# Optimization experiments

Measured on AMD Instinct MI355X. Metric: run time of the kernel, lower is better.

Reference implementation:

```python
import jax, jax.numpy as jnp
import numpy as np
from jax.scipy.special import gammaln

# sizes (see shape_source)
N_CELLS = 1024
N_GENES = 1000
N_LATENT = 50
NB_ENC = 16          # encoder histogram bins per gene
NB_DEC = 16          # decoder mixture components (sum(n_decoder_bins))
N_HID = 16           # encoder hidden dim
N_CUTS = 4_000_000
N_FRAGS = 2_000_000
N_TOTAL_CELLS = 10_000
N_TOTAL_CUTS = 50_000_000
BN_EPS = 1e-5


def _normal_logprob(x, loc, scale):
    z = (x - loc) / scale
    return -0.5 * z * z - jnp.log(scale) - 0.5 * jnp.log(2.0 * jnp.pi)


def setup_inputs() -> dict:
    key = jax.random.key(0)
    ks = jax.random.split(key, 20)
    cut_coordinates = jax.random.uniform(ks[0], (N_CUTS,), dtype=jnp.float32)
    cut_cell = jax.random.randint(ks[1], (N_CUTS,), 0, N_CELLS)
    cut_local_gene_ix = jax.random.randint(ks[2], (N_CUTS,), 0, N_GENES)
    cut_local_cellxgene_ix = cut_cell * N_GENES + cut_local_gene_ix
    local_cellxgene_ix = jax.random.randint(ks[3], (N_FRAGS,), 0, N_CELLS * N_GENES)
    genes_oi = jnp.arange(N_GENES)
    cells_oi = jnp.arange(N_CELLS)
    eps = jax.random.normal(ks[4], (N_CELLS, N_LATENT), dtype=jnp.float32)
    n_in = N_GENES * NB_ENC
    enc_W1 = jax.random.normal(ks[5], (n_in, N_HID)) * (1.0 / np.sqrt(n_in))
    enc_b1 = jnp.zeros((N_HID,))
    bn_gamma = jnp.ones((N_HID,))
    bn_beta = jnp.zeros((N_HID,))
    W_loc = jax.random.normal(ks[6], (N_HID, N_LATENT)) * (1.0 / np.sqrt(N_HID))
    b_loc = jnp.zeros((N_LATENT,))
    W_scale = jax.random.normal(ks[7], (N_HID, N_LATENT)) * (1.0 / np.sqrt(N_HID))
    b_scale = jnp.zeros((N_LATENT,))
    logit_weight = jax.random.normal(ks[8], (N_GENES, N_LATENT, NB_DEC)) * 0.05
    rho_weight = jax.random.normal(ks[9], (N_GENES, N_LATENT)) * 0.05
    baseline_heights = jax.random.normal(ks[10], (N_GENES, NB_DEC)) * 0.1
    libsize = jax.random.randint(ks[11], (N_TOTAL_CELLS,), 1000, 20000)
    rho_bias = jax.random.uniform(ks[12], (N_GENES,), minval=1e-4, maxval=1e-2)
    return dict(
        cut_coordinates=cut_coordinates, eps=eps,
        enc_W1=enc_W1, enc_b1=enc_b1, bn_gamma=bn_gamma, bn_beta=bn_beta,
        W_loc=W_loc, b_loc=b_loc, W_scale=W_scale, b_scale=b_scale,
        logit_weight=logit_weight, rho_weight=rho_weight,
        baseline_heights=baseline_heights, rho_bias=rho_bias,
        cut_local_cellxgene_ix=cut_local_cellxgene_ix,
        cut_local_gene_ix=cut_local_gene_ix,
        local_cellxgene_ix=local_cellxgene_ix,
        genes_oi=genes_oi, cells_oi=cells_oi, libsize=libsize,
    )


def reference(cut_coordinates, eps, enc_W1, enc_b1, bn_gamma, bn_beta,
              W_loc, b_loc, W_scale, b_scale, logit_weight, rho_weight,
              baseline_heights, rho_bias, cut_local_cellxgene_ix,
              cut_local_gene_ix, local_cellxgene_ix, genes_oi, cells_oi,
              libsize):
    n_cells = cells_oi.shape[0]
    n_genes = genes_oi.shape[0]

    # ---- Encoder: digitize + bincount histogram ----
    bin_enc = jnp.minimum(jnp.floor(cut_coordinates * NB_ENC), NB_ENC - 1).astype(jnp.int32)
    digitized = bin_enc + cut_local_cellxgene_ix.astype(jnp.int32) * NB_ENC
    counts = jax.ops.segment_sum(jnp.ones_like(cut_coordinates), digitized,
                                 num_segments=n_cells * n_genes * NB_ENC)
    x = jnp.log1p(counts.reshape(n_cells, n_genes * NB_ENC))  # [C, G*NB]

    h = x @ enc_W1 + enc_b1
    mu = h.mean(axis=0)
    var = h.var(axis=0)  # biased, matches torch BN in train mode
    h = (h - mu) / jnp.sqrt(var + BN_EPS) * bn_gamma + bn_beta
    h = jax.nn.relu(h)
    loc = h @ W_loc + b_loc                 # [C, L]
    scale = jnp.exp(h @ W_scale + b_scale)  # [C, L]

    # ---- latent sample + KL ----
    q_scale = scale * 0.1
    latent = loc + q_scale * eps
    latent_kl = (_normal_logprob(latent, 0.0, 1.0)
                 - _normal_logprob(latent, loc, q_scale)) * (N_TOTAL_CELLS / n_cells)

    # ---- Decoder (n_layers=0: per-gene linear heads) ----
    lw = logit_weight[genes_oi]                       # [G, L, K]
    rw = rho_weight[genes_oi]                         # [G, L]
    mixture_delta = jnp.einsum('cl,glk->cgk', latent, lw)  # [C, G, K]
    rho_delta = jnp.einsum('cl,gl->cg', latent, rw)        # [C, G]
    md_cxg = mixture_delta.reshape(n_cells * n_genes, NB_DEC)
    md_cut = md_cxg[cut_local_cellxgene_ix]           # [N_CUTS, K] gather
    mixture_delta_kl = _normal_logprob(lw, 0.0, 0.1)

    # ---- mixture likelihood: piecewise-constant spline density per cut ----
    logits = baseline_heights[cut_local_gene_ix] + md_cut  # [N_CUTS, K]
    logp = jax.nn.log_softmax(logits, axis=-1)
    bin_dec = jnp.minimum(jnp.floor(cut_coordinates * NB_DEC), NB_DEC - 1).astype(jnp.int32)
    likelihood_mixture = (jnp.take_along_axis(logp, bin_dec[:, None], axis=1)[:, 0]
                          + jnp.log(float(NB_DEC)))

    # ---- fragment-count Poisson likelihood ----
    fragexpr = (rho_bias[genes_oi][None, :] * jnp.exp(rho_delta)
                * libsize[cells_oi].astype(jnp.float32)[:, None])  # [C, G]
    fragmentcounts = jax.ops.segment_sum(
        jnp.ones((local_cellxgene_ix.shape[0],), jnp.float32),
        local_cellxgene_ix, num_segments=n_cells * n_genes
    ).reshape(n_cells, n_genes)
    likelihood_frag = (fragmentcounts * jnp.log(fragexpr) - fragexpr
                       - gammaln(fragmentcounts + 1.0))

    rho_delta_kl = _normal_logprob(rw, 0.0, 0.1)

    likelihood = (likelihood_mixture.sum() * (N_TOTAL_CUTS / cut_coordinates.shape[0])
                  + likelihood_frag.sum() * (N_TOTAL_CELLS / n_cells))
    elbo = (-likelihood - latent_kl.sum() - mixture_delta_kl.sum()
            - rho_delta_kl.sum())
    return elbo
```

## Files before the change

kernel.cpp:

```cpp
#include <hip/hip_runtime.h>
#include <hip/hip_bf16.h>
#include <math.h>


#define G_      1000
#define C_      1024
#define L_      50
#define K_      16
#define NHID_   16
#define CUT_SCALE   12.5f
#define CELL_SCALE  9.765625f

#define CHUNK_    6144
#define RCAP_CUT  18432
#define RCAP_FRAG 9216

#define NPB_MIX  4000
#define NPB_POIS 4000
#define NPB_WKL  256
#define NPB_TOT  8456

#define GCNTC_OFF  0ull
#define GCNTF_OFF  1024ull
#define ZERO_BYTES 2048ull
#define BNSUM_OFF  2048ull
#define LATBF_OFF  2304ull
#define LWT_OFF    133376ull
#define ENTC_OFF   2181376ull
#define ENTF_OFF   11618560ull
#define MERGED_OFF 16337152ull
#define FRAGU8_OFF 24529152ull
#define P_OFF      25577728ull
#define HT_OFF     29772032ull
#define LATT_OFF   29837568ull
#define PB_OFF     30042368ull
#define WS_NEED    30076192ull

typedef __attribute__((ext_vector_type(8))) short short8;
typedef __attribute__((ext_vector_type(4))) float f32x4;

__device__ __constant__ float LGT[32] = {
    0.0f, 0.0f, 0.6931471805599453f, 1.791759469228055f, 3.1780538303479458f,
    4.787491742782046f, 6.579251212010101f, 8.525161361065415f,
    10.60460290274525f, 12.801827480081469f, 15.104412573075516f,
    17.502307845873887f, 19.987214495661885f, 22.552163853123425f,
    25.19122118273868f, 27.89927138384089f, 30.671860106080672f,
    33.50507345013689f, 36.39544520803305f, 39.339884187199495f,
    42.335616460753485f, 45.38013889847691f, 48.47118135183523f,
    51.60667556776438f, 54.78472939811232f, 58.00360522298052f,
    61.261701761002f, 64.55753862700633f, 67.88974313718154f,
    71.25703896716801f, 74.65823634883016f, 78.0922235533153f };

__device__ __forceinline__ float block_sum_256(float v) {
    __shared__ float sm[256];
    int t = threadIdx.x;
    __syncthreads();
    sm[t] = v;
    __syncthreads();
#pragma unroll
    for (int s = 128; s > 0; s >>= 1) {
        if (t < s) sm[t] += sm[t + s];
        __syncthreads();
    }
    return sm[0];
}

__global__ __launch_bounds__(256)
void part_kernel(const int* __restrict__ cut_ix,
                 const float* __restrict__ coord,
                 const int* __restrict__ frag_ix,
                 unsigned int* __restrict__ gcnt_c,
                 unsigned int* __restrict__ gcnt_f,
                 unsigned short* __restrict__ entc,
                 unsigned short* __restrict__ entf,
                 const float* __restrict__ lw,
                 const float* __restrict__ rw,
                 __hip_bfloat16* __restrict__ lwT,
                 float* __restrict__ pb_wkl,
                 int n_cuts, int n_frags, int ncc, int nblk_part) {
    int t = threadIdx.x;
    int bid = blockIdx.x;
    if (bid >= nblk_part) {
        int r = bid - nblk_part;
        if (r < 256) {
            for (int g = r; g < G_; g += 256) {
                for (int i = t; i < L_ * K_; i += 256) {
                    float v = lw[(size_t)g * (L_ * K_) + i];
                    lwT[(size_t)g * 1024 + (i & 15) * 64 + (i >> 4)] =
                        __float2bfloat16(v);
                }
                for (int i = t; i < 16 * 14; i += 256) {
                    int n = i / 14, l = 50 + (i % 14);
                    lwT[(size_t)g * 1024 + n * 64 + l] = __float2bfloat16(0.f);
                }
            }
        } else {
            const int NTOT = G_ * L_ * K_ + G_ * L_;
            int wb = r - 256;
            float s = 0.f;
            for (int i = wb * 256 + t; i < NTOT; i += 256 * 256) {
                float w = (i < G_ * L_ * K_) ? lw[i] : rw[i - G_ * L_ * K_];
                s += fmaf(-50.f * w, w, 1.3836465597893733f);
            }
            s = block_sum_256(s);
            if (t == 0) pb_wkl[wb] = -s;
        }
        return;
    }
    __shared__ unsigned int cnt[256], excl[256], cur[256], gbas[256];
    __shared__ unsigned short stage[CHUNK_];
    __shared__ unsigned char bkof[CHUNK_];
    bool isCut = (bid < ncc);
    int blk = isCut ? bid : bid - ncc;
    const int* idx = isCut ? cut_ix : frag_ix;
    int n = isCut ? n_cuts : n_frags;
    int rcap = isCut ? RCAP_CUT : RCAP_FRAG;
    unsigned int* gcount = isCut ? gcnt_c : gcnt_f;
    unsigned short* ent = isCut ? entc : entf;
    int i0 = blk * CHUNK_;
    cnt[t] = 0;
    int4 I[6]; float4 X[6];
    unsigned int vm;
    bool full = (i0 + CHUNK_ <= n);
    if (full) {
        const int4* ip = (const int4*)(idx + i0);
#pragma unroll
        for (int k = 0; k < 6; ++k) I[k] = ip[k * 256 + t];
        if (isCut) {
            const float4* xp = (const float4*)(coord + i0);
#pragma unroll
            for (int k = 0; k < 6; ++k) X[k] = xp[k * 256 + t];
        }
        vm = 0xFFFFFFu;
    } else {
        vm = 0;
#pragma unroll
        for (int k = 0; k < 6; ++k) {
            int r0 = i0 + (k * 256 + t) * 4;
            int* Ii = (int*)&I[k]; float* Xi = (float*)&X[k];
#pragma unroll
            for (int u = 0; u < 4; ++u) {
                bool v = (r0 + u) < n;
                if (v) vm |= 1u << (k * 4 + u);
                Ii[u] = v ? idx[r0 + u] : 0;
                Xi[u] = (v && isCut) ? coord[r0 + u] : 0.f;
            }
        }
    }
    __syncthreads();
#pragma unroll
    for (int k = 0; k < 6; ++k) {
        const int* Ii = (const int*)&I[k];
        const float* Xi = (const float*)&X[k];
#pragma unroll
        for (int u = 0; u < 4; ++u) {
            if (vm & (1u << (k * 4 + u))) {
                int ix = Ii[u];
                int c = ix / G_;
                int g = ix - c * G_;
                unsigned int bk;
                if (isCut) {
                    int b = (int)(Xi[u] * 16.f); b = b > 15 ? 15 : b;
                    bk = ((unsigned)(c >> 6) << 4) | ((unsigned)(g * K_ + b) >> 10);
                } else {
                    bk = ((unsigned)(c >> 6) << 4) | ((unsigned)g >> 6);
                }
                atomicAdd(&cnt[bk], 1u);
            }
        }
    }
    __syncthreads();
    excl[t] = cnt[t];
    __syncthreads();
    for (int o = 1; o < 256; o <<= 1) {
        unsigned int v = (t >= o) ? excl[t - o] : 0u;
        __syncthreads();
        excl[t] += v;
        __syncthreads();
    }
    unsigned int my_excl = excl[t] - cnt[t];
    gbas[t] = cnt[t] ? atomicAdd(&gcount[t], cnt[t]) : 0u;
    cur[t] = my_excl;
    __syncthreads();
    excl[t] = my_excl;
    __syncthreads();
#pragma unroll
    for (int k = 0; k < 6; ++k) {
        const int* Ii = (const int*)&I[k];
        const float* Xi = (const float*)&X[k];
#pragma unroll
        for (int u = 0; u < 4; ++u) {
            if (vm & (1u << (k * 4 + u))) {
                int ix = Ii[u];
                int c = ix / G_;
                int g = ix - c * G_;
                unsigned int bk; unsigned short e;
                if (isCut) {
                    int b = (int)(Xi[u] * 16.f); b = b > 15 ? 15 : b;
                    int bin = g * K_ + b;
                    bk = ((unsigned)(c >> 6) << 4) | ((unsigned)bin >> 10);
                    e = (unsigned short)(((c & 63) << 10) | (bin & 1023));
                } else {
                    bk = ((unsigned)(c >> 6) << 4) | ((unsigned)g >> 6);
                    e = (unsigned short)(((c & 63) << 6) | (g & 63));
                }
                unsigned int p = atomicAdd(&cur[bk], 1u);
                stage[p] = e;
                bkof[p] = (unsigned char)bk;
            }
        }
    }
    __syncthreads();
    int total = n - i0; if (total > CHUNK_) total = CHUNK_;
    for (int p = t; p < total; p += 256) {
        unsigned int bk = bkof[p];
        unsigned int dst = gbas[bk] + (p - excl[bk]);
        if (dst < (unsigned)rcap)
            ent[(size_t)bk * rcap + dst] = stage[p];
    }
}

__global__ __launch_bounds__(256)
void mid_kernel(const unsigned int* __restrict__ gcnt_c,
                const unsigned short* __restrict__ entc,
                const unsigned int* __restrict__ gcnt_f,
                const unsigned short* __restrict__ entf,
                const float* __restrict__ W1,
                unsigned int* __restrict__ merged,
                unsigned int* __restrict__ fragw,
                float* __restrict__ P) {
    __shared__ unsigned int h[4096];
    __shared__ float w1s[4096];
    int t = threadIdx.x;
    int bid = blockIdx.x;
    if (bid < 1024) {
        int bk = bid >> 2, q = bid & 3;
        int cg = bk >> 4, bc = bk & 15;
        int wbase = (bc * 1024 + q * 256) * NHID_;
#pragma unroll
        for (int r = 0; r < 16; ++r) {
            int i = r * 256 + t;
            int gi = wbase + i;
            w1s[i] = (gi < 16000 * NHID_) ? W1[gi] : 0.f;
        }
        for (int i = t; i < 2048; i += 256) h[i] = 0;
        __syncthreads();
        unsigned int count = gcnt_c[bk];
        if (count > RCAP_CUT) count = RCAP_CUT;
        const unsigned int* e32 = (const unsigned int*)(entc + (size_t)bk * RCAP_CUT);
        unsigned int npair = count >> 1;
        for (unsigned int base = 0; base < npair; base += 1024) {
            unsigned int w[4]; bool val[4];
#pragma unroll
            for (int u = 0; u < 4; ++u) {
                unsigned int p = base + u * 256 + t;
                val[u] = (p < npair);
                w[u] = val[u] ? e32[p] : 0u;
            }
#pragma unroll
            for (int u = 0; u < 4; ++u) {
                if (val[u]) {
                    unsigned int v0 = w[u] & 0xffffu, v1 = w[u] >> 16;
                    unsigned int b0 = v0 & 1023u, b1 = v1 & 1023u;
                    if ((int)(b0 >> 8) == q) {
                        unsigned int c0 = v0 >> 10;
                        atomicAdd(&h[(b0 & 255u) * 8 + (c0 >> 3)],
                                  1u << ((c0 & 7) * 4));
                    }
                    if ((int)(b1 >> 8) == q) {
                        unsigned int c1 = v1 >> 10;
                        atomicAdd(&h[(b1 & 255u) * 8 + (c1 >> 3)],
                                  1u << ((c1 & 7) * 4));
                    }
                }
            }
        }
        if (t == 0 && (count & 1u)) {
            unsigned int v = ((const unsigned short*)e32)[count - 1];
            unsigned int b0 = v & 1023u;
            if ((int)(b0 >> 8) == q) {
                unsigned int c0 = v >> 10;
                atomicAdd(&h[(b0 & 255u) * 8 + (c0 >> 3)], 1u << ((c0 & 7) * 4));
            }
        }
        __syncthreads();
        for (int i = t; i < 2048; i += 256) {
            int bin = bc * 1024 + q * 256 + (i >> 3);
            if (bin < 16000)
                merged[(unsigned)bin * 128u + (unsigned)cg * 8u + (i & 7)] = h[i];
        }
        int c_lo = t & 63, sub = t >> 6;
        float acc[NHID_];
#pragma unroll
        for (int j = 0; j < NHID_; ++j) acc[j] = 0.f;
        int rbase = bc * 1024 + q * 256 + sub * 64;
        int sh = (c_lo & 7) * 4;
        const float4* w1v = (const float4*)w1s;
#pragma unroll 2
        for (int bl = 0; bl < 64; ++bl) {
            int row = rbase + bl;
            if (row < 16000) {
                int rl = sub * 64 + bl;
                unsigned int w = h[rl * 8 + (c_lo >> 3)];
                float xv = __logf((float)(((w >> sh) & 0xfu) + 1u));
                float4 wa = w1v[rl * 4 + 0];
                float4 wb = w1v[rl * 4 + 1];
                float4 wc = w1v[rl * 4 + 2];
                float4 wd = w1v[rl * 4 + 3];
                acc[0] = fmaf(xv, wa.x, acc[0]);  acc[1] = fmaf(xv, wa.y, acc[1]);
                acc[2] = fmaf(xv, wa.z, acc[2]);  acc[3] = fmaf(xv, wa.w, acc[3]);
                acc[4] = fmaf(xv, wb.x, acc[4]);  acc[5] = fmaf(xv, wb.y, acc[5]);
                acc[6] = fmaf(xv, wb.z, acc[6]);  acc[7] = fmaf(xv, wb.w, acc[7]);
                acc[8] = fmaf(xv, wc.x, acc[8]);  acc[9] = fmaf(xv, wc.y, acc[9]);
                acc[10] = fmaf(xv, wc.z, acc[10]); acc[11] = fmaf(xv, wc.w, acc[11]);
                acc[12] = fmaf(xv, wd.x, acc[12]); acc[13] = fmaf(xv, wd.y, acc[13]);
                acc[14] = fmaf(xv, wd.z, acc[14]); acc[15] = fmaf(xv, wd.w, acc[15]);
            }
        }
        __syncthreads();
        float* sp = (float*)h;
#pragma unroll
        for (int j = 0; j < NHID_; ++j) sp[sub * 1024 + j * 64 + c_lo] = acc[j];
        __syncthreads();
        for (int i = t; i < 1024; i += 256) {
            int j = i >> 6, c = i & 63;
            float v = sp[j * 64 + c] + sp[1024 + j * 64 + c]
                    + sp[2048 + j * 64 + c] + sp[3072 + j * 64 + c];
            P[(size_t)((bc * 4 + q) * NHID_ + j) * C_ + cg * 64 + c] = v;
        }
    } else {
        int bk = bid - 1024, cg = bk >> 4, gc = bk & 15;
        for (int i = t; i < 2048; i += 256) h[i] = 0;
        __syncthreads();
        unsigned int count = gcnt_f[bk];
        if (count > RCAP_FRAG) count = RCAP_FRAG;
        const unsigned short* e = entf + (size_t)bk * RCAP_FRAG;
#pragma unroll 4
        for (unsigned int p = t; p < count; p += 256) {
            unsigned int v = e[p];
            unsigned int g_lo = v & 63u;
            unsigned int c_lo = v >> 6;
            atomicAdd(&h[g_lo * 32 + (c_lo >> 1)], 1u << ((c_lo & 1) * 16));
        }
        __syncthreads();
        for (int i = t; i < 1024; i += 256) {
            int g_lo = i >> 4, wb = i & 15;
            unsigned int lo = h[g_lo * 32 + wb * 2];
            unsigned int hi = h[g_lo * 32 + wb * 2 + 1];
            unsigned int outv = (lo & 0xffu) | (((lo >> 16) & 0xffu) << 8)
                              | ((hi & 0xffu) << 16) | (((hi >> 16) & 0xffu) << 24);
            int g = gc * 64 + g_lo;
            if (g < G_)
                fragw[(unsigned)g * 256u + (unsigned)cg * 16u + wb] = outv;
        }
    }
}

__global__ __launch_bounds__(256)
void bn_kernel(const float* __restrict__ P,
               float* __restrict__ hT,
               double* __restrict__ bnsum) {
    int j = blockIdx.x;
    int t = threadIdx.x;
    float s1 = 0.f, s2 = 0.f;
#pragma unroll
    for (int u = 0; u < 4; ++u) {
        int c = u * 256 + t;
        float s = 0.f;
#pragma unroll 8
        for (int ch = 0; ch < 64; ++ch)
            s += P[(size_t)(ch * NHID_ + j) * C_ + c];
        hT[j * C_ + c] = s;
        s1 += s; s2 += s * s;
    }
    s1 = block_sum_256(s1);
    s2 = block_sum_256(s2);
    if (t == 0) { bnsum[j] = (double)s1; bnsum[NHID_ + j] = (double)s2; }
}

__global__ __launch_bounds__(256)
void latent_kernel(const float* __restrict__ hT,
                   const double* __restrict__ bnsum,
                   const float* __restrict__ gamma,
                   const float* __restrict__ beta,
                   const float* __restrict__ W_loc,
                   const float* __restrict__ b_loc,
                   const float* __restrict__ W_scale,
                   const float* __restrict__ b_scale,
                   const float* __restrict__ eps,
                   float* __restrict__ latT,
                   __hip_bfloat16* __restrict__ latbf,
                   float* __restrict__ pb) {
    int idx = blockIdx.x * 256 + threadIdx.x;
    float kl = 0.f;
    {
        int c = idx / L_;
        int l = idx - c * L_;
        float hb[NHID_];
#pragma unroll
        for (int j = 0; j < NHID_; ++j) {
            float mean = (float)(bnsum[j] * (1.0 / C_));
            float ex2  = (float)(bnsum[NHID_ + j] * (1.0 / C_));
            float var = ex2 - mean * mean;
            float rstd = rsqrtf(var + 1e-5f);
            float sc = gamma[j] * rstd;
            float sh = beta[j] - mean * sc;
            float v = fmaf(hT[j * C_ + c], sc, sh);
            hb[j] = v > 0.f ? v : 0.f;
        }
        float loc = b_loc[l], ls = b_scale[l];
#pragma unroll
        for (int j = 0; j < NHID_; ++j) {
            loc = fmaf(hb[j], W_loc[j * L_ + l], loc);
            ls  = fmaf(hb[j], W_scale[j * L_ + l], ls);
        }
        float qs = 0.1f * __expf(ls);
        float e = eps[idx];
        float lat = fmaf(qs, e, loc);
        latT[(size_t)l * C_ + c] = lat;
        latbf[c * 64 + l] = __float2bfloat16(lat);
        if (l < 14) latbf[c * 64 + 50 + l] = __float2bfloat16(0.f);
        float z = (lat - loc) / qs;
        kl = fmaf(-0.5f * lat, lat, fmaf(0.5f * z, z, __logf(qs)));
    }
    float s = block_sum_256(kl);
    if (threadIdx.x == 0) pb[blockIdx.x] = -CELL_SCALE * s;
}

__global__ __launch_bounds__(256)
void mixpois_kernel(const __hip_bfloat16* __restrict__ latbf,
                    const __hip_bfloat16* __restrict__ lwT,
                    const unsigned int* __restrict__ merged,
                    const float* __restrict__ baseline,
                    const float* __restrict__ latT,
                    const float* __restrict__ rw,
                    const float* __restrict__ rho_bias,
                    const int* __restrict__ libsize,
                    const unsigned char* __restrict__ fragb,
                    float* __restrict__ pb) {
    int g = blockIdx.x;
    if (blockIdx.y < 4) {
        int lane = threadIdx.x & 63;
        int wv = threadIdx.x >> 6;
        int n = lane & 15;
        int quad = lane >> 4;
        const __hip_bfloat16* bb = lwT + (size_t)g * 1024 + n * 64 + quad * 8;
        short8 b1 = *(const short8*)bb;
        short8 b2 = *(const short8*)(bb + 32);
        float bl = baseline[g * K_ + n];
        float partial = 0.f;
        int cwave = blockIdx.y * 256 + wv * 64;
#pragma unroll
        for (int mt = 0; mt < 4; ++mt) {
            int c0 = cwave + mt * 16;
            const __hip_bfloat16* aa = latbf + (size_t)(c0 + n) * 64 + quad * 8;
            short8 a1 = *(const short8*)aa;
            short8 a2 = *(const short8*)(aa + 32);
            f32x4 d = {bl, bl, bl, bl};
            d = __builtin_amdgcn_mfma_f32_16x16x32_bf16(a1, b1, d, 0, 0, 0);
            d = __builtin_amdgcn_mfma_f32_16x16x32_bf16(a2, b2, d, 0, 0, 0);
            float mx[4], ex[4];
#pragma unroll
            for (int r = 0; r < 4; ++r) mx[r] = d[r];
#pragma unroll
            for (int m = 1; m < 16; m <<= 1)
#pragma unroll
                for (int r = 0; r < 4; ++r)
                    mx[r] = fmaxf(mx[r], __shfl_xor(mx[r], m));
#pragma unroll
            for (int r = 0; r < 4; ++r) ex[r] = __expf(d[r] - mx[r]);
#pragma unroll
            for (int m = 1; m < 16; m <<= 1)
#pragma unroll
                for (int r = 0; r < 4; ++r) ex[r] += __shfl_xor(ex[r], m);
            int cp = c0 + quad * 4;
            unsigned int hw =
                merged[(unsigned)(g * K_ + n) * 128u + ((unsigned)cp >> 3)];
            int sb = (cp & 7) * 4;
#pragma unroll
            for (int r = 0; r < 4; ++r) {
                float lse = mx[r] + __logf(ex[r]);
                float cnt = (float)((hw >> (sb + r * 4)) & 0xfu);
                partial = fmaf(cnt, d[r] - lse, partial);
            }
        }
        float s = block_sum_256(-CUT_SCALE * partial);
        if (threadIdx.x == 0) pb[blockIdx.y * G_ + g] = s;
    } else {
        int yc = blockIdx.y - 4;
        int c = yc * 256 + threadIdx.x;
        const float* rwg = rw + (size_t)g * L_;
        float rho = 0.f;
#pragma unroll 10
        for (int l = 0; l < L_; ++l)
            rho = fmaf(latT[l * C_ + c], rwg[l], rho);
        unsigned int fc = fragb[(size_t)g * C_ + c];
        float fe = rho_bias[g] * __expf(rho) * (float)libsize[c];
        float lf = fmaf((float)fc, __logf(fe), -fe) - LGT[fc > 31u ? 31u : fc];
        float s = block_sum_256(-CELL_SCALE * lf);
        if (threadIdx.x == 0) pb[NPB_MIX + yc * G_ + g] = s;
    }
}

__global__ __launch_bounds__(256)
void final_kernel(const float* __restrict__ pb, float* __restrict__ out) {
    __shared__ double sm[256];
    int t = threadIdx.x;
    double a = 0.0;
    for (int i = t; i < NPB_TOT; i += 256) a += (double)pb[i];
    sm[t] = a;
    __syncthreads();
#pragma unroll
    for (int s = 128; s > 0; s >>= 1) {
        if (t < s) sm[t] += sm[t + s];
        __syncthreads();
    }
    if (t == 0) out[0] = (float)(sm[0] - 138629436.11198905);
}

extern "C" void kernel_launch(void* const* d_in, const int* in_sizes, int n_in,
                              void* d_out, int out_size, void* d_ws, size_t ws_size,
                              hipStream_t stream) {
    const float* cut_coord = (const float*)d_in[0];
    const float* eps       = (const float*)d_in[1];
    const float* enc_W1    = (const float*)d_in[2];
    const float* bn_gamma  = (const float*)d_in[4];
    const float* bn_beta   = (const float*)d_in[5];
    const float* W_loc     = (const float*)d_in[6];
    const float* b_loc     = (const float*)d_in[7];
    const float* W_scale   = (const float*)d_in[8];
    const float* b_scale   = (const float*)d_in[9];
    const float* logit_w   = (const float*)d_in[10];
    const float* rho_w     = (const float*)d_in[11];
    const float* baseline  = (const float*)d_in[12];
    const float* rho_bias  = (const float*)d_in[13];
    const int* cut_cxg     = (const int*)d_in[14];
    const int* frag_ix     = (const int*)d_in[16];
    const int* libsize     = (const int*)d_in[19];

    int n_cuts  = in_sizes[0];
    int n_frags = in_sizes[16];

    char* ws = (char*)d_ws;
    unsigned int*   gcnt_c = (unsigned int*)(ws + GCNTC_OFF);
    unsigned int*   gcnt_f = (unsigned int*)(ws + GCNTF_OFF);
    double*         bnsum  = (double*)(ws + BNSUM_OFF);
    __hip_bfloat16* latbf  = (__hip_bfloat16*)(ws + LATBF_OFF);
    __hip_bfloat16* lwT    = (__hip_bfloat16*)(ws + LWT_OFF);
    unsigned short* entc   = (unsigned short*)(ws + ENTC_OFF);
    unsigned short* entf   = (unsigned short*)(ws + ENTF_OFF);
    unsigned int*   merged = (unsigned int*)(ws + MERGED_OFF);
    unsigned int*   fragw  = (unsigned int*)(ws + FRAGU8_OFF);
    float*          P      = (float*)(ws + P_OFF);
    float*          hT     = (float*)(ws + HT_OFF);
    float*          latT   = (float*)(ws + LATT_OFF);
    float*          pb     = (float*)(ws + PB_OFF);
    float*          out    = (float*)d_out;

    int ncc = (n_cuts + CHUNK_ - 1) / CHUNK_;
    int ncf = (n_frags + CHUNK_ - 1) / CHUNK_;
    int nblk_part = ncc + ncf;

    hipMemsetAsync(ws, 0, ZERO_BYTES, stream);

    part_kernel<<<nblk_part + 512, 256, 0, stream>>>(
        cut_cxg, cut_coord, frag_ix, gcnt_c, gcnt_f, entc, entf,
        logit_w, rho_w, lwT, pb + NPB_MIX + NPB_POIS,
        n_cuts, n_frags, ncc, nblk_part);
    mid_kernel<<<1280, 256, 0, stream>>>(
        gcnt_c, entc, gcnt_f, entf, enc_W1, merged, fragw, P);
    bn_kernel<<<NHID_, 256, 0, stream>>>(P, hT, bnsum);
    latent_kernel<<<(C_ * L_) / 256, 256, 0, stream>>>(
        hT, bnsum, bn_gamma, bn_beta, W_loc, b_loc, W_scale, b_scale,
        eps, latT, latbf, pb + NPB_MIX + NPB_POIS + NPB_WKL);
    mixpois_kernel<<<dim3(G_, 8), 256, 0, stream>>>(
        latbf, lwT, merged, baseline, latT, rho_w, rho_bias, libsize,
        (const unsigned char*)fragw, pb);
    final_kernel<<<1, 256, 0, stream>>>(pb, out);
}
```

Baseline: 244.6 us.

## Fold BN and final reduction into neighbouring kernels; atomic-accumulate encoder hidden sums

Removes bn_kernel by having mid_kernel atomically add its partial hidden activations straight into hT, and each latent_kernel block recomputes the batch-norm statistics itself. final_kernel is merged into mixpois_kernel using a two-level done counter, so the last block performs the final sum. The bucket prefix scan becomes a wavefront shuffle scan, and W1 is read from global memory with a wave-uniform address instead of being staged in LDS. The changes cut kernel launches, the P round trip and LDS usage. In exchange they add float atomics with nondeterministic summation order, redundant BN statistics work in every latent block, and a last-block completion protocol.

After: 369.5 us. 1.51x slower.

```diff
diff --git a/kernel.cpp b/kernel.cpp
--- a/kernel.cpp
+++ b/kernel.cpp
@@ -22,19 +22,18 @@
 
 #define GCNTC_OFF  0ull
 #define GCNTF_OFF  1024ull
-#define ZERO_BYTES 2048ull
-#define BNSUM_OFF  2048ull
-#define LATBF_OFF  2304ull
-#define LWT_OFF    133376ull
-#define ENTC_OFF   2181376ull
-#define ENTF_OFF   11618560ull
-#define MERGED_OFF 16337152ull
-#define FRAGU8_OFF 24529152ull
-#define P_OFF      25577728ull
-#define HT_OFF     29772032ull
-#define LATT_OFF   29837568ull
-#define PB_OFF     30042368ull
-#define WS_NEED    30076192ull
+#define DONE_OFF   2048ull
+#define HT_OFF     18688ull
+#define ZERO_BYTES 84224ull
+#define LATBF_OFF  84224ull
+#define LWT_OFF    215296ull
+#define ENTC_OFF   2263296ull
+#define ENTF_OFF   11700480ull
+#define MERGED_OFF 16419072ull
+#define FRAGU8_OFF 24611072ull
+#define LATT_OFF   25635072ull
+#define PB_OFF     25839872ull
+#define WS_NEED    25873696ull
 
 typedef __attribute__((ext_vector_type(8))) short short8;
 typedef __attribute__((ext_vector_type(4))) float f32x4;
@@ -170,19 +169,25 @@
         }
     }
     __syncthreads();
-    excl[t] = cnt[t];
-    __syncthreads();
-    for (int o = 1; o < 256; o <<= 1) {
-        unsigned int v = (t >= o) ? excl[t - o] : 0u;
-        __syncthreads();
-        excl[t] += v;
-        __syncthreads();
-    }
-    unsigned int my_excl = excl[t] - cnt[t];
+    if (t < 64) {
+        unsigned int c0 = cnt[t * 4 + 0], c1 = cnt[t * 4 + 1];
+        unsigned int c2 = cnt[t * 4 + 2], c3 = cnt[t * 4 + 3];
+        unsigned int tot = c0 + c1 + c2 + c3;
+        unsigned int run = tot;
+#pragma unroll
+        for (int o = 1; o < 64; o <<= 1) {
+            unsigned int v = __shfl_up(run, o, 64);
+            if (t >= o) run += v;
+        }
+        unsigned int base = run - tot;
+        excl[t * 4 + 0] = base;
+        excl[t * 4 + 1] = base + c0;
+        excl[t * 4 + 2] = base + c0 + c1;
+        excl[t * 4 + 3] = base + c0 + c1 + c2;
+    }
+    __syncthreads();
     gbas[t] = cnt[t] ? atomicAdd(&gcount[t], cnt[t]) : 0u;
-    cur[t] = my_excl;
-    __syncthreads();
-    excl[t] = my_excl;
+    cur[t] = excl[t];
     __syncthreads();
 #pragma unroll
     for (int k = 0; k < 6; ++k) {
@@ -228,21 +233,13 @@
                 const float* __restrict__ W1,
                 unsigned int* __restrict__ merged,
                 unsigned int* __restrict__ fragw,
-                float* __restrict__ P) {
+                float* __restrict__ hT) {
     __shared__ unsigned int h[4096];
-    __shared__ float w1s[4096];
     int t = threadIdx.x;
     int bid = blockIdx.x;
     if (bid < 1024) {
         int bk = bid >> 2, q = bid & 3;
         int cg = bk >> 4, bc = bk & 15;
-        int wbase = (bc * 1024 + q * 256) * NHID_;
-#pragma unroll
-        for (int r = 0; r < 16; ++r) {
-            int i = r * 256 + t;
-            int gi = wbase + i;
-            w1s[i] = (gi < 16000 * NHID_) ? W1[gi] : 0.f;
-        }
         for (int i = t; i < 2048; i += 256) h[i] = 0;
         __syncthreads();
         unsigned int count = gcnt_c[bk];
@@ -295,7 +292,6 @@
         for (int j = 0; j < NHID_; ++j) acc[j] = 0.f;
         int rbase = bc * 1024 + q * 256 + sub * 64;
         int sh = (c_lo & 7) * 4;
-        const float4* w1v = (const float4*)w1s;
 #pragma unroll 2
         for (int bl = 0; bl < 64; ++bl) {
             int row = rbase + bl;
@@ -303,10 +299,12 @@
                 int rl = sub * 64 + bl;
                 unsigned int w = h[rl * 8 + (c_lo >> 3)];
                 float xv = __logf((float)(((w >> sh) & 0xfu) + 1u));
-                float4 wa = w1v[rl * 4 + 0];
-                float4 wb = w1v[rl * 4 + 1];
-                float4 wc = w1v[rl * 4 + 2];
-                float4 wd = w1v[rl * 4 + 3];
+                const float4* wr = (const float4*)
+                    (W1 + (size_t)__builtin_amdgcn_readfirstlane(row) * NHID_);
+                float4 wa = wr[0];
+                float4 wb = wr[1];
+                float4 wc = wr[2];
+                float4 wd = wr[3];
                 acc[0] = fmaf(xv, wa.x, acc[0]);  acc[1] = fmaf(xv, wa.y, acc[1]);
                 acc[2] = fmaf(xv, wa.z, acc[2]);  acc[3] = fmaf(xv, wa.w, acc[3]);
                 acc[4] = fmaf(xv, wb.x, acc[4]);  acc[5] = fmaf(xv, wb.y, acc[5]);
@@ -326,7 +324,7 @@
             int j = i >> 6, c = i & 63;
             float v = sp[j * 64 + c] + sp[1024 + j * 64 + c]
                     + sp[2048 + j * 64 + c] + sp[3072 + j * 64 + c];
-            P[(size_t)((bc * 4 + q) * NHID_ + j) * C_ + cg * 64 + c] = v;
+            atomicAdd(&hT[j * C_ + cg * 64 + c], v);
         }
     } else {
         int bk = bid - 1024, cg = bk >> 4, gc = bk & 15;
@@ -357,30 +355,7 @@
 }
 
 __global__ __launch_bounds__(256)
-void bn_kernel(const float* __restrict__ P,
-               float* __restrict__ hT,
-               double* __restrict__ bnsum) {
-    int j = blockIdx.x;
-    int t = threadIdx.x;
-    float s1 = 0.f, s2 = 0.f;
-#pragma unroll
-    for (int u = 0; u < 4; ++u) {
-        int c = u * 256 + t;
-        float s = 0.f;
-#pragma unroll 8
-        for (int ch = 0; ch < 64; ++ch)
-            s += P[(size_t)(ch * NHID_ + j) * C_ + c];
-        hT[j * C_ + c] = s;
-        s1 += s; s2 += s * s;
-    }
-    s1 = block_sum_256(s1);
-    s2 = block_sum_256(s2);
-    if (t == 0) { bnsum[j] = (double)s1; bnsum[NHID_ + j] = (double)s2; }
-}
-
-__global__ __launch_bounds__(256)
 void latent_kernel(const float* __restrict__ hT,
-                   const double* __restrict__ bnsum,
                    const float* __restrict__ gamma,
                    const float* __restrict__ beta,
                    const float* __restrict__ W_loc,
@@ -391,7 +366,32 @@
                    float* __restrict__ latT,
                    __hip_bfloat16* __restrict__ latbf,
                    float* __restrict__ pb) {
-    int idx = blockIdx.x * 256 + threadIdx.x;
+    __shared__ float scs[NHID_], shs[NHID_];
+    int t = threadIdx.x;
+    {
+        int j = t >> 4, cl = t & 15;
+        double s1 = 0.0, s2 = 0.0;
+#pragma unroll 8
+        for (int k = 0; k < 64; ++k) {
+            float v = hT[j * C_ + cl + k * 16];
+            s1 += (double)v; s2 += (double)v * (double)v;
+        }
+#pragma unroll
+        for (int m = 1; m < 16; m <<= 1) {
+            s1 += __shfl_xor(s1, m);
+            s2 += __shfl_xor(s2, m);
+        }
+        if (cl == 0) {
+            double mean = s1 * (1.0 / C_);
+            double var = s2 * (1.0 / C_) - mean * mean;
+            float rstd = rsqrtf((float)var + 1e-5f);
+            float sc = gamma[j] * rstd;
+            scs[j] = sc;
+            shs[j] = beta[j] - (float)mean * sc;
+        }
+    }
+    __syncthreads();
+    int idx = blockIdx.x * 256 + t;
     float kl = 0.f;
     {
         int c = idx / L_;
@@ -399,13 +399,7 @@
         float hb[NHID_];
 #pragma unroll
         for (int j = 0; j < NHID_; ++j) {
-            float mean = (float)(bnsum[j] * (1.0 / C_));
-            float ex2  = (float)(bnsum[NHID_ + j] * (1.0 / C_));
-            float var = ex2 - mean * mean;
-            float rstd = rsqrtf(var + 1e-5f);
-            float sc = gamma[j] * rstd;
-            float sh = beta[j] - mean * sc;
-            float v = fmaf(hT[j * C_ + c], sc, sh);
+            float v = fmaf(hT[j * C_ + c], scs[j], shs[j]);
             hb[j] = v > 0.f ? v : 0.f;
         }
         float loc = b_loc[l], ls = b_scale[l];
@@ -437,7 +431,9 @@
                     const float* __restrict__ rho_bias,
                     const int* __restrict__ libsize,
                     const unsigned char* __restrict__ fragb,
-                    float* __restrict__ pb) {
+                    float* __restrict__ pb,
+                    unsigned int* __restrict__ done,
+                    float* __restrict__ out) {
     int g = blockIdx.x;
     if (blockIdx.y < 4) {
         int lane = threadIdx.x & 63;
@@ -500,22 +496,33 @@
         float s = block_sum_256(-CELL_SCALE * lf);
         if (threadIdx.x == 0) pb[NPB_MIX + yc * G_ + g] = s;
     }
-}
-
-__global__ __launch_bounds__(256)
-void final_kernel(const float* __restrict__ pb, float* __restrict__ out) {
-    __shared__ double sm[256];
-    int t = threadIdx.x;
-    double a = 0.0;
-    for (int i = t; i < NPB_TOT; i += 256) a += (double)pb[i];
-    sm[t] = a;
-    __syncthreads();
-#pragma unroll
-    for (int s = 128; s > 0; s >>= 1) {
-        if (t < s) sm[t] += sm[t + s];
-        __syncthreads();
-    }
-    if (t == 0) out[0] = (float)(sm[0] - 138629436.11198905);
+    __shared__ int lastflag;
+    if (threadIdx.x == 0) {
+        lastflag = 0;
+        __threadfence();
+        int s = blockIdx.x & 63;
+        unsigned int quota = ((s < 40) ? 16u : 15u) * 8u;
+        if (atomicAdd(&done[s * 64], 1u) == quota - 1u) {
+            __threadfence();
+            if (atomicAdd(&done[4096], 1u) == 63u) lastflag = 1;
+        }
+    }
+    __syncthreads();
+    if (lastflag) {
+        __threadfence();
+        __shared__ double smd[256];
+        int t = threadIdx.x;
+        double a = 0.0;
+        for (int i = t; i < NPB_TOT; i += 256) a += (double)pb[i];
+        smd[t] = a;
+        __syncthreads();
+#pragma unroll
+        for (int s2 = 128; s2 > 0; s2 >>= 1) {
+            if (t < s2) smd[t] += smd[t + s2];
+            __syncthreads();
+        }
+        if (t == 0) out[0] = (float)(smd[0] - 138629436.11198905);
+    }
 }
 
 extern "C" void kernel_launch(void* const* d_in, const int* in_sizes, int n_in,
@@ -544,15 +551,14 @@
     char* ws = (char*)d_ws;
     unsigned int*   gcnt_c = (unsigned int*)(ws + GCNTC_OFF);
     unsigned int*   gcnt_f = (unsigned int*)(ws + GCNTF_OFF);
-    double*         bnsum  = (double*)(ws + BNSUM_OFF);
+    unsigned int*   done   = (unsigned int*)(ws + DONE_OFF);
+    float*          hT     = (float*)(ws + HT_OFF);
     __hip_bfloat16* latbf  = (__hip_bfloat16*)(ws + LATBF_OFF);
     __hip_bfloat16* lwT    = (__hip_bfloat16*)(ws + LWT_OFF);
     unsigned short* entc   = (unsigned short*)(ws + ENTC_OFF);
     unsigned short* entf   = (unsigned short*)(ws + ENTF_OFF);
     unsigned int*   merged = (unsigned int*)(ws + MERGED_OFF);
     unsigned int*   fragw  = (unsigned int*)(ws + FRAGU8_OFF);
-    float*          P      = (float*)(ws + P_OFF);
-    float*          hT     = (float*)(ws + HT_OFF);
     float*          latT   = (float*)(ws + LATT_OFF);
     float*          pb     = (float*)(ws + PB_OFF);
     float*          out    = (float*)d_out;
@@ -568,13 +574,11 @@
         logit_w, rho_w, lwT, pb + NPB_MIX + NPB_POIS,
         n_cuts, n_frags, ncc, nblk_part);
     mid_kernel<<<1280, 256, 0, stream>>>(
-        gcnt_c, entc, gcnt_f, entf, enc_W1, merged, fragw, P);
-    bn_kernel<<<NHID_, 256, 0, stream>>>(P, hT, bnsum);
+        gcnt_c, entc, gcnt_f, entf, enc_W1, merged, fragw, hT);
     latent_kernel<<<(C_ * L_) / 256, 256, 0, stream>>>(
-        hT, bnsum, bn_gamma, bn_beta, W_loc, b_loc, W_scale, b_scale,
+        hT, bn_gamma, bn_beta, W_loc, b_loc, W_scale, b_scale,
         eps, latT, latbf, pb + NPB_MIX + NPB_POIS + NPB_WKL);
     mixpois_kernel<<<dim3(G_, 8), 256, 0, stream>>>(
         latbf, lwT, merged, baseline, latT, rho_w, rho_bias, libsize,
-        (const unsigned char*)fragw, pb);
-    final_kernel<<<1, 256, 0, stream>>>(pb, out);
+        (const unsigned char*)fragw, pb, done, out);
 }
```
